# Performance work log

Hardware: AMD Instinct MI355X
Metric: run time of the kernel (lower is better)

The kernel has to match this reference:

```python
import jax, jax.numpy as jnp
import numpy as np

H = 1024          # hidden_dim
E = 8             # num_experts
TOP_K = 2
FF = 4 * H        # ExpertFFN inner dim (standard transformer FFN assumption)
B, S = 2, 2048


def setup_inputs() -> dict:
    key = jax.random.key(0)
    ks = jax.random.split(key, 12)
    std = 0.02 / np.sqrt(H)
    return {
        "x": jax.random.normal(ks[0], (B, S, H), dtype=jnp.float32),
        "gate_w": jax.random.normal(ks[1], (E, H), dtype=jnp.float32) * std,  # nn.Linear weight [out,in]
        "gate_b": jnp.zeros((E,), dtype=jnp.float32),                          # self.bias param
        # routed experts, stacked: FFN = W2 @ gelu(W1 @ x + b1) + b2
        "w1": jax.random.normal(ks[2], (E, H, FF), dtype=jnp.float32) * (1.0 / np.sqrt(H)),
        "b1": jnp.zeros((E, FF), dtype=jnp.float32),
        "w2": jax.random.normal(ks[3], (E, FF, H), dtype=jnp.float32) * (1.0 / np.sqrt(FF)),
        "b2": jnp.zeros((E, H), dtype=jnp.float32),
        # shared expert
        "sw1": jax.random.normal(ks[4], (H, FF), dtype=jnp.float32) * (1.0 / np.sqrt(H)),
        "sb1": jnp.zeros((FF,), dtype=jnp.float32),
        "sw2": jax.random.normal(ks[5], (FF, H), dtype=jnp.float32) * (1.0 / np.sqrt(FF)),
        "sb2": jnp.zeros((H,), dtype=jnp.float32),
    }


def _moe_forward(x, gate_w, gate_b, w1, b1, w2, b2, sw1, sb1, sw2, sb2):
    b, s, h = x.shape
    xf = x.reshape(-1, h)                                    # [T, H]
    # sigmoid gating with learned bias (aux-loss-free load balancing bias)
    scores = jax.nn.sigmoid(xf @ gate_w.T + gate_b)          # [T, E]
    top_scores, top_idx = jax.lax.top_k(scores, TOP_K)       # [T, k]
    top_scores = top_scores / (top_scores.sum(-1, keepdims=True) + 1e-6)
    # per-expert combine weights: sum of normalized scores over top-k slots
    comb = (jax.nn.one_hot(top_idx, E, dtype=xf.dtype) * top_scores[..., None]).sum(1)  # [T, E]
    # dense grouped FFN over all experts (reference; faithful math to masked dispatch)
    hdn = jax.nn.gelu(jnp.einsum('th,ehf->etf', xf, w1) + b1[:, None, :], approximate=False)
    y = jnp.einsum('etf,efh->eth', hdn, w2) + b2[:, None, :]  # [E, T, H]
    routed = jnp.einsum('te,eth->th', comb, y)                # [T, H]
    shared = (jax.nn.gelu(xf @ sw1 + sb1, approximate=False) @ sw2 + sb2) * 0.1
    return (routed + shared).reshape(b, s, h)                 # dropout: eval mode (identity)


def reference(x, gate_w, gate_b, w1, b1, w2, b2, sw1, sb1, sw2, sb2):
    return _moe_forward(x, gate_w, gate_b, w1, b1, w2, b2, sw1, sb1, sw2, sb2)
```

## Files before the change

kernel.cpp:

```cpp
#include <hip/hip_runtime.h>
#include <stdint.h>

#define H_DIM 1024
#define E_NUM 8
#define FF_DIM 4096
#define T_TOK 4096

typedef __bf16 bf16x8 __attribute__((ext_vector_type(8)));
typedef float f32x4 __attribute__((ext_vector_type(4)));

#define AS1 __attribute__((address_space(1)))
#define AS3 __attribute__((address_space(3)))

__device__ __forceinline__ unsigned short f2bf(float f) {
  union { float f; uint32_t u; } v; v.f = f;
  uint32_t u = v.u;
  uint32_t r = u + 0x7fffu + ((u >> 16) & 1u);
  return (unsigned short)(r >> 16);
}
__device__ __forceinline__ float bf2f(unsigned short u) {
  union { uint32_t u; float f; } v; v.u = ((uint32_t)u) << 16;
  return v.f;
}

__device__ __forceinline__ float gelu_f(float x) {
  float s = x * x;
  float g = x * (1.5957691216f + 0.0713548162f * s);
  float t = __expf(-g);
  return x * __builtin_amdgcn_rcpf(1.0f + t);
}

#define GATE_BLOCKS (T_TOK / 4)
#define W1T_BLOCKS (64 * 16 * (E_NUM + 1))
__global__ __launch_bounds__(256) void gate_w1t_kernel(
    const float* __restrict__ x, const float* __restrict__ gw, const float* __restrict__ gb,
    int* __restrict__ topidx, float* __restrict__ topw, int* __restrict__ counts,
    unsigned short* __restrict__ xb,
    const float* __restrict__ w1, const float* __restrict__ sw1,
    unsigned short* __restrict__ w1t) {
  __shared__ float tile[64][65];
  const int bid = blockIdx.x;

  if (bid < GATE_BLOCKS) {
    const int t = bid * 4 + (threadIdx.x >> 6);
    const int l = threadIdx.x & 63;
    const float* xt = x + (size_t)t * H_DIM;
    float acc[E_NUM];
    #pragma unroll
    for (int e = 0; e < E_NUM; e++) acc[e] = 0.f;
    for (int k = l; k < H_DIM; k += 64) {
      float xv = xt[k];
      #pragma unroll
      for (int e = 0; e < E_NUM; e++) acc[e] += xv * gw[e * H_DIM + k];
    }
    unsigned short* xrow = xb + (size_t)t * H_DIM;
    #pragma unroll
    for (int i = 0; i < 4; i++) {
      int idx = l + i * 64;
      float4 v = *(const float4*)(xt + idx * 4);
      ushort4 o;
      o.x = f2bf(v.x); o.y = f2bf(v.y); o.z = f2bf(v.z); o.w = f2bf(v.w);
      *(ushort4*)(xrow + idx * 4) = o;
    }
    #pragma unroll
    for (int e = 0; e < E_NUM; e++) {
      float v = acc[e];
      #pragma unroll
      for (int off = 32; off > 0; off >>= 1) v += __shfl_xor(v, off, 64);
      acc[e] = v;
    }
    if (l == 0) {
      float s[E_NUM];
      #pragma unroll
      for (int e = 0; e < E_NUM; e++) s[e] = 1.f / (1.f + __expf(-(acc[e] + gb[e])));
      int i1 = 0; float v1 = s[0];
      #pragma unroll
      for (int e = 1; e < E_NUM; e++) if (s[e] > v1) { v1 = s[e]; i1 = e; }
      int i2 = -1; float v2 = -1.f;
      #pragma unroll
      for (int e = 0; e < E_NUM; e++) if (e != i1 && s[e] > v2) { v2 = s[e]; i2 = e; }
      float denom = v1 + v2 + 1e-6f;
      topidx[t * 2]     = i1; topidx[t * 2 + 1] = i2;
      topw[t * 2]       = v1 / denom;
      topw[t * 2 + 1]   = v2 / denom;
      atomicAdd(&counts[i1], 1);
      atomicAdd(&counts[i2], 1);
    }
    return;
  }

  const int tb  = bid - GATE_BLOCKS;
  const int z   = tb >> 10;
  const int rem = tb & 1023;
  const int c0 = (rem & 63) * 64;
  const int r0 = (rem >> 6) * 64;
  const float* inb = (z < E_NUM) ? (w1 + (size_t)z * H_DIM * FF_DIM) : sw1;
  unsigned short* outb = w1t + (size_t)z * H_DIM * FF_DIM;
  const int tx = threadIdx.x & 15, ty = threadIdx.x >> 4;
  #pragma unroll
  for (int i = 0; i < 4; i++) {
    int row = ty + i * 16;
    float4 v = *(const float4*)(inb + (size_t)(r0 + row) * FF_DIM + c0 + tx * 4);
    tile[row][tx * 4 + 0] = v.x;
    tile[row][tx * 4 + 1] = v.y;
    tile[row][tx * 4 + 2] = v.z;
    tile[row][tx * 4 + 3] = v.w;
  }
  __syncthreads();
  int rr0 = tx * 4;
  #pragma unroll
  for (int p = 0; p < 4; p++) {
    int col = p * 16 + ty;
    ushort4 o;
    o.x = f2bf(tile[rr0 + 0][col]);
    o.y = f2bf(tile[rr0 + 1][col]);
    o.z = f2bf(tile[rr0 + 2][col]);
    o.w = f2bf(tile[rr0 + 3][col]);
    *(ushort4*)(outb + (size_t)(c0 + col) * H_DIM + r0 + rr0) = o;
  }
}

__global__ void scan_kernel(const int* __restrict__ counts, int* __restrict__ offs,
                            int* __restrict__ cursor) {
  if (threadIdx.x == 0) {
    int a = 0;
    for (int e = 0; e < E_NUM; e++) { offs[e] = a; a += counts[e]; cursor[e] = 0; }
    offs[E_NUM] = a;
    offs[E_NUM + 1] = a + T_TOK;
  }
}

__global__ void dispatch_kernel(const int* __restrict__ topidx,
                                const int* __restrict__ offs, int* __restrict__ cursor,
                                int* __restrict__ gidx, int* __restrict__ slot_of) {
  int t = blockIdx.x * blockDim.x + threadIdx.x;
  if (t >= T_TOK) return;
  #pragma unroll
  for (int j = 0; j < 2; j++) {
    int ex  = topidx[t * 2 + j];
    int pos = atomicAdd(&cursor[ex], 1);
    int slot = offs[ex] + pos;
    gidx[slot] = t;
    slot_of[t * 2 + j] = slot;
  }
}

template <bool FFN1>
__global__ __launch_bounds__(256, 4) void gemm64x256(
    const unsigned short* __restrict__ A,
    const unsigned short* __restrict__ Bt,
    const float* __restrict__ b_r,
    const float* __restrict__ b_s,
    unsigned short* __restrict__ outp,
    const int* __restrict__ offs,
    const int* __restrict__ gidx,
    const float* __restrict__ w2src,
    const float* __restrict__ sw2src,
    unsigned short* __restrict__ w2t,
    int K, int N) {
  __shared__ __align__(16) char ldsA[64 * 128];
  __shared__ __align__(16) char ldsB[256 * 128];

  if (FFN1 && blockIdx.z == E_NUM + 1) {
    float (*tile)[65] = (float (*)[65])ldsB;
    const int c0 = blockIdx.x * 64;
    const int r0 = blockIdx.y * 64;
    const int tx = threadIdx.x & 15, ty = threadIdx.x >> 4;
    for (int z2 = 0; z2 <= E_NUM; z2++) {
      const float* inb = (z2 < E_NUM) ? (w2src + (size_t)z2 * FF_DIM * H_DIM) : sw2src;
      unsigned short* outb = w2t + (size_t)z2 * FF_DIM * H_DIM;
      #pragma unroll
      for (int i = 0; i < 4; i++) {
        int row = ty + i * 16;
        float4 v = *(const float4*)(inb + (size_t)(r0 + row) * H_DIM + c0 + tx * 4);
        tile[row][tx * 4 + 0] = v.x;
        tile[row][tx * 4 + 1] = v.y;
        tile[row][tx * 4 + 2] = v.z;
        tile[row][tx * 4 + 3] = v.w;
      }
      __syncthreads();
      int rr0 = tx * 4;
      #pragma unroll
      for (int p = 0; p < 4; p++) {
        int col = p * 16 + ty;
        ushort4 o;
        o.x = f2bf(tile[rr0 + 0][col]);
        o.y = f2bf(tile[rr0 + 1][col]);
        o.z = f2bf(tile[rr0 + 2][col]);
        o.w = f2bf(tile[rr0 + 3][col]);
        *(ushort4*)(outb + (size_t)(c0 + col) * FF_DIM + r0 + rr0) = o;
      }
      __syncthreads();
    }
    return;
  }

  const int e  = blockIdx.z;
  const int m0 = blockIdx.y * 64;
  const int cnt = offs[e + 1] - offs[e];
  if (m0 >= cnt) return;
  const int base  = offs[e] + m0;
  const int valid = min(64, cnt - m0);
  const int slotMax = offs[e] + cnt - 1;
  const int n0 = blockIdx.x * 256;

  const int tid = threadIdx.x;
  const int l = tid & 63;

  const int srow = tid >> 3;
  const int su   = (tid & 7) ^ (srow & 7);
  const unsigned short* aSrc[2];
  const unsigned short* bSrc[8];
  const unsigned short* BtE = Bt + (size_t)e * (size_t)N * (size_t)K;
  #pragma unroll
  for (int j = 0; j < 2; j++) {
    int slot = base + j * 32 + srow;
    size_t arow;
    if (FFN1) {
      int tok = (e < E_NUM) ? gidx[min(slot, slotMax)] : (slot - 2 * T_TOK);
      arow = (size_t)tok;
    } else {
      arow = (size_t)slot;
    }
    aSrc[j] = A + arow * (size_t)K + su * 8;
  }
  #pragma unroll
  for (int j = 0; j < 8; j++) {
    int r = j * 32 + srow;
    int rr = r & 63;
    int nr = n0 + (r & 192) + ((rr & 15) << 2) + (rr >> 4);
    bSrc[j] = BtE + (size_t)nr * (size_t)K + su * 8;
  }

  f32x4 acc[4][4];
  #pragma unroll
  for (int m = 0; m < 4; m++)
    #pragma unroll
    for (int n = 0; n < 4; n++) acc[m][n] = (f32x4){0.f, 0.f, 0.f, 0.f};

  const int wc = tid >> 6;
  const int l15 = l & 15, l4 = l >> 4, l7 = l & 7;

  for (int kt = 0; kt < K; kt += 64) {
    #pragma unroll
    for (int j = 0; j < 2; j++)
      __builtin_amdgcn_global_load_lds((const AS1 void*)(aSrc[j] + kt),
                                       (AS3 void*)(ldsA + (j * 256 + tid) * 16), 16, 0, 0);
    #pragma unroll
    for (int j = 0; j < 8; j++)
      __builtin_amdgcn_global_load_lds((const AS1 void*)(bSrc[j] + kt),
                                       (AS3 void*)(ldsB + (j * 256 + tid) * 16), 16, 0, 0);
    __syncthreads();
    #pragma unroll
    for (int kk = 0; kk < 2; kk++) {
      const int uoff = ((kk * 4 + l4) ^ l7) << 4;
      bf16x8 af[4], bfr[4];
      #pragma unroll
      for (int m = 0; m < 4; m++)
        af[m] = *(const bf16x8*)(ldsA + (m * 16 + l15) * 128 + uoff);
      #pragma unroll
      for (int n = 0; n < 4; n++)
        bfr[n] = *(const bf16x8*)(ldsB + (wc * 64 + n * 16 + l15) * 128 + uoff);
      #pragma unroll
      for (int m = 0; m < 4; m++)
        #pragma unroll
        for (int n = 0; n < 4; n++)
          acc[m][n] = __builtin_amdgcn_mfma_f32_16x16x32_bf16(af[m], bfr[n], acc[m][n], 0, 0, 0);
    }
    __syncthreads();
  }

  const float* bias = (e < E_NUM) ? (b_r + (size_t)e * N) : b_s;
  const int c0 = n0 + wc * 64 + 4 * l15;
  float4 bv = *(const float4*)(bias + c0);
  #pragma unroll
  for (int m = 0; m < 4; m++) {
    #pragma unroll
    for (int j = 0; j < 4; j++) {
      int rl = m * 16 + l4 * 4 + j;
      if (rl < valid) {
        ushort4 o;
        if (FFN1) {
          o.x = f2bf(gelu_f(acc[m][0][j] + bv.x));
          o.y = f2bf(gelu_f(acc[m][1][j] + bv.y));
          o.z = f2bf(gelu_f(acc[m][2][j] + bv.z));
          o.w = f2bf(gelu_f(acc[m][3][j] + bv.w));
        } else {
          o.x = f2bf(acc[m][0][j] + bv.x);
          o.y = f2bf(acc[m][1][j] + bv.y);
          o.z = f2bf(acc[m][2][j] + bv.z);
          o.w = f2bf(acc[m][3][j] + bv.w);
        }
        *(ushort4*)(outp + (size_t)(base + rl) * N + c0) = o;
      }
    }
  }
}

__global__ __launch_bounds__(256) void combine_kernel(
    const unsigned short* __restrict__ y, const float* __restrict__ topw,
    const int* __restrict__ slot_of, float* __restrict__ out) {
  int t = blockIdx.x;
  int g = threadIdx.x;
  int s1 = slot_of[2 * t], s2 = slot_of[2 * t + 1];
  float w1 = topw[2 * t], w2 = topw[2 * t + 1];
  ushort4 a = *(const ushort4*)(y + (size_t)s1 * H_DIM + g * 4);
  ushort4 b = *(const ushort4*)(y + (size_t)s2 * H_DIM + g * 4);
  ushort4 c = *(const ushort4*)(y + (size_t)(2 * T_TOK + t) * H_DIM + g * 4);
  float4 o;
  o.x = w1 * bf2f(a.x) + w2 * bf2f(b.x) + 0.1f * bf2f(c.x);
  o.y = w1 * bf2f(a.y) + w2 * bf2f(b.y) + 0.1f * bf2f(c.y);
  o.z = w1 * bf2f(a.z) + w2 * bf2f(b.z) + 0.1f * bf2f(c.z);
  o.w = w1 * bf2f(a.w) + w2 * bf2f(b.w) + 0.1f * bf2f(c.w);
  *(float4*)(out + (size_t)t * H_DIM + g * 4) = o;
}

extern "C" void kernel_launch(void* const* d_in, const int* in_sizes, int n_in,
                              void* d_out, int out_size, void* d_ws, size_t ws_size,
                              hipStream_t stream) {
  const float* x   = (const float*)d_in[0];
  const float* gw  = (const float*)d_in[1];
  const float* gb  = (const float*)d_in[2];
  const float* w1  = (const float*)d_in[3];
  const float* b1  = (const float*)d_in[4];
  const float* w2  = (const float*)d_in[5];
  const float* b2  = (const float*)d_in[6];
  const float* sw1 = (const float*)d_in[7];
  const float* sb1 = (const float*)d_in[8];
  const float* sw2 = (const float*)d_in[9];
  const float* sb2 = (const float*)d_in[10];
  float* out = (float*)d_out;

  char* p = (char*)d_ws;
  auto alloc = [&](size_t bytes) {
    char* r = p;
    p += (bytes + 255) & ~(size_t)255;
    return r;
  };
  int*   counts  = (int*)alloc(E_NUM * 4);
  int*   cursor  = (int*)alloc(E_NUM * 4);
  int*   offs    = (int*)alloc((E_NUM + 2) * 4);
  int*   topidx  = (int*)alloc((size_t)T_TOK * 2 * 4);
  float* topw    = (float*)alloc((size_t)T_TOK * 2 * 4);
  int*   slot_of = (int*)alloc((size_t)T_TOK * 2 * 4);
  int*   gidx    = (int*)alloc((size_t)2 * T_TOK * 4);
  unsigned short* xb    = (unsigned short*)alloc((size_t)T_TOK * H_DIM * 2);
  unsigned short* wAll1 = (unsigned short*)alloc((size_t)(E_NUM + 1) * FF_DIM * H_DIM * 2);
  unsigned short* wAll2 = (unsigned short*)alloc((size_t)(E_NUM + 1) * FF_DIM * H_DIM * 2);
  unsigned short* hdn   = (unsigned short*)alloc((size_t)3 * T_TOK * FF_DIM * 2);
  unsigned short* yb    = (unsigned short*)alloc((size_t)3 * T_TOK * H_DIM * 2);

  hipMemsetAsync(counts, 0, E_NUM * 4, stream);

  gate_w1t_kernel<<<GATE_BLOCKS + W1T_BLOCKS, 256, 0, stream>>>(
      x, gw, gb, topidx, topw, counts, xb, w1, sw1, wAll1);
  scan_kernel<<<1, 1, 0, stream>>>(counts, offs, cursor);
  dispatch_kernel<<<T_TOK / 256, 256, 0, stream>>>(topidx, offs, cursor, gidx, slot_of);

  gemm64x256<true><<<dim3(FF_DIM / 256, T_TOK / 64, E_NUM + 2), 256, 0, stream>>>(
      xb, wAll1, b1, sb1, hdn, offs, gidx, w2, sw2, wAll2, H_DIM, FF_DIM);

  gemm64x256<false><<<dim3(H_DIM / 256, T_TOK / 64, E_NUM + 1), 256, 0, stream>>>(
      hdn, wAll2, b2, sb2, yb, offs, nullptr, nullptr, nullptr, nullptr, FF_DIM, H_DIM);

  combine_kernel<<<T_TOK, 256, 0, stream>>>(yb, topw, slot_of, out);
}
```

Measured before the change: 494.5 us.

## Fuse weighted combine into FFN2 epilogue via float atomic scatter-add

Removes the separate combine kernel and the bf16 intermediate y buffer. The FFN2 GEMM epilogue now scales each row by its routing weight (or 0.1 for shared) and atomically adds into the zero-initialized fp32 output at the token row. Dispatch stores per-slot weights instead of slot indices. This saves a kernel launch and a write/read of y, but adds a memset of the output and scalar fp32 atomics (three contributions per output element), which can contend and make summation order nondeterministic.

```diff
diff --git a/kernel.cpp b/kernel.cpp
--- a/kernel.cpp
+++ b/kernel.cpp
@@ -17,10 +17,6 @@
   uint32_t u = v.u;
   uint32_t r = u + 0x7fffu + ((u >> 16) & 1u);
   return (unsigned short)(r >> 16);
-}
-__device__ __forceinline__ float bf2f(unsigned short u) {
-  union { uint32_t u; float f; } v; v.u = ((uint32_t)u) << 16;
-  return v.f;
 }
 
 __device__ __forceinline__ float gelu_f(float x) {
@@ -130,9 +126,9 @@
   }
 }
 
-__global__ void dispatch_kernel(const int* __restrict__ topidx,
+__global__ void dispatch_kernel(const int* __restrict__ topidx, const float* __restrict__ topw,
                                 const int* __restrict__ offs, int* __restrict__ cursor,
-                                int* __restrict__ gidx, int* __restrict__ slot_of) {
+                                int* __restrict__ gidx, float* __restrict__ gwt) {
   int t = blockIdx.x * blockDim.x + threadIdx.x;
   if (t >= T_TOK) return;
   #pragma unroll
@@ -141,7 +137,7 @@
     int pos = atomicAdd(&cursor[ex], 1);
     int slot = offs[ex] + pos;
     gidx[slot] = t;
-    slot_of[t * 2 + j] = slot;
+    gwt[slot]  = topw[t * 2 + j];
   }
 }
 
@@ -151,9 +147,10 @@
     const unsigned short* __restrict__ Bt,
     const float* __restrict__ b_r,
     const float* __restrict__ b_s,
-    unsigned short* __restrict__ outp,
+    void* __restrict__ outp,
     const int* __restrict__ offs,
     const int* __restrict__ gidx,
+    const float* __restrict__ gwt,
     const float* __restrict__ w2src,
     const float* __restrict__ sw2src,
     unsigned short* __restrict__ w2t,
@@ -279,40 +276,27 @@
     for (int j = 0; j < 4; j++) {
       int rl = m * 16 + l4 * 4 + j;
       if (rl < valid) {
-        ushort4 o;
         if (FFN1) {
+          ushort4 o;
           o.x = f2bf(gelu_f(acc[m][0][j] + bv.x));
           o.y = f2bf(gelu_f(acc[m][1][j] + bv.y));
           o.z = f2bf(gelu_f(acc[m][2][j] + bv.z));
           o.w = f2bf(gelu_f(acc[m][3][j] + bv.w));
+          *(ushort4*)((unsigned short*)outp + (size_t)(base + rl) * N + c0) = o;
         } else {
-          o.x = f2bf(acc[m][0][j] + bv.x);
-          o.y = f2bf(acc[m][1][j] + bv.y);
-          o.z = f2bf(acc[m][2][j] + bv.z);
-          o.w = f2bf(acc[m][3][j] + bv.w);
+          int slot = base + rl;
+          int tok; float w;
+          if (e < E_NUM) { tok = gidx[slot]; w = gwt[slot]; }
+          else           { tok = slot - 2 * T_TOK; w = 0.1f; }
+          float* orow = (float*)outp + (size_t)tok * N + c0;
+          atomicAdd(orow + 0, w * (acc[m][0][j] + bv.x));
+          atomicAdd(orow + 1, w * (acc[m][1][j] + bv.y));
+          atomicAdd(orow + 2, w * (acc[m][2][j] + bv.z));
+          atomicAdd(orow + 3, w * (acc[m][3][j] + bv.w));
         }
-        *(ushort4*)(outp + (size_t)(base + rl) * N + c0) = o;
       }
     }
   }
-}
-
-__global__ __launch_bounds__(256) void combine_kernel(
-    const unsigned short* __restrict__ y, const float* __restrict__ topw,
-    const int* __restrict__ slot_of, float* __restrict__ out) {
-  int t = blockIdx.x;
-  int g = threadIdx.x;
-  int s1 = slot_of[2 * t], s2 = slot_of[2 * t + 1];
-  float w1 = topw[2 * t], w2 = topw[2 * t + 1];
-  ushort4 a = *(const ushort4*)(y + (size_t)s1 * H_DIM + g * 4);
-  ushort4 b = *(const ushort4*)(y + (size_t)s2 * H_DIM + g * 4);
-  ushort4 c = *(const ushort4*)(y + (size_t)(2 * T_TOK + t) * H_DIM + g * 4);
-  float4 o;
-  o.x = w1 * bf2f(a.x) + w2 * bf2f(b.x) + 0.1f * bf2f(c.x);
-  o.y = w1 * bf2f(a.y) + w2 * bf2f(b.y) + 0.1f * bf2f(c.y);
-  o.z = w1 * bf2f(a.z) + w2 * bf2f(b.z) + 0.1f * bf2f(c.z);
-  o.w = w1 * bf2f(a.w) + w2 * bf2f(b.w) + 0.1f * bf2f(c.w);
-  *(float4*)(out + (size_t)t * H_DIM + g * 4) = o;
 }
 
 extern "C" void kernel_launch(void* const* d_in, const int* in_sizes, int n_in,
@@ -342,26 +326,24 @@
   int*   offs    = (int*)alloc((E_NUM + 2) * 4);
   int*   topidx  = (int*)alloc((size_t)T_TOK * 2 * 4);
   float* topw    = (float*)alloc((size_t)T_TOK * 2 * 4);
-  int*   slot_of = (int*)alloc((size_t)T_TOK * 2 * 4);
   int*   gidx    = (int*)alloc((size_t)2 * T_TOK * 4);
+  float* gwt     = (float*)alloc((size_t)2 * T_TOK * 4);
   unsigned short* xb    = (unsigned short*)alloc((size_t)T_TOK * H_DIM * 2);
   unsigned short* wAll1 = (unsigned short*)alloc((size_t)(E_NUM + 1) * FF_DIM * H_DIM * 2);
   unsigned short* wAll2 = (unsigned short*)alloc((size_t)(E_NUM + 1) * FF_DIM * H_DIM * 2);
   unsigned short* hdn   = (unsigned short*)alloc((size_t)3 * T_TOK * FF_DIM * 2);
-  unsigned short* yb    = (unsigned short*)alloc((size_t)3 * T_TOK * H_DIM * 2);
 
   hipMemsetAsync(counts, 0, E_NUM * 4, stream);
+  hipMemsetAsync(out, 0, (size_t)T_TOK * H_DIM * 4, stream);
 
   gate_w1t_kernel<<<GATE_BLOCKS + W1T_BLOCKS, 256, 0, stream>>>(
       x, gw, gb, topidx, topw, counts, xb, w1, sw1, wAll1);
   scan_kernel<<<1, 1, 0, stream>>>(counts, offs, cursor);
-  dispatch_kernel<<<T_TOK / 256, 256, 0, stream>>>(topidx, offs, cursor, gidx, slot_of);
+  dispatch_kernel<<<T_TOK / 256, 256, 0, stream>>>(topidx, topw, offs, cursor, gidx, gwt);
 
   gemm64x256<true><<<dim3(FF_DIM / 256, T_TOK / 64, E_NUM + 2), 256, 0, stream>>>(
-      xb, wAll1, b1, sb1, hdn, offs, gidx, w2, sw2, wAll2, H_DIM, FF_DIM);
+      xb, wAll1, b1, sb1, hdn, offs, gidx, gwt, w2, sw2, wAll2, H_DIM, FF_DIM);
 
   gemm64x256<false><<<dim3(H_DIM / 256, T_TOK / 64, E_NUM + 1), 256, 0, stream>>>(
-      hdn, wAll2, b2, sb2, yb, offs, nullptr, nullptr, nullptr, nullptr, FF_DIM, H_DIM);
-
-  combine_kernel<<<T_TOK, 256, 0, stream>>>(yb, topw, slot_of, out);
-}
+      hdn, wAll2, b2, sb2, out, offs, gidx, gwt, nullptr, nullptr, nullptr, FF_DIM, H_DIM);
+}
```

After: 608.9 us. 23.1% more time.
